# Kernel tuning notes

Measured on AMD Instinct MI355X. Metric: run time of the kernel, lower is better.

The kernel has to match this reference:

```python
import jax, jax.numpy as jnp
import numpy as np
from jax import lax
from jax.scipy.special import logsumexp

B, T, K, D = 16, 128, 1024, 768
APPROX_R = 0.1
LAMBD = 0.1
KP = int(APPROX_R * K)  # num_state_approx = 102


def setup_inputs() -> dict:
    key = jax.random.key(0)
    k0, k1, k2, k3 = jax.random.split(key, 4)
    x_emb = jax.random.normal(k0, (B, T, D), jnp.float32)
    # nn.Parameter(torch.normal(0, norm_scale_transition, [K, D]))
    state_matrix = 0.01 * jax.random.normal(k1, (K, D), jnp.float32)
    y = jax.random.randint(k2, (B, T), 0, K)
    y_lens = jax.random.randint(k3, (B,), 1, T + 1)
    return {"x_emb": x_emb, "state_matrix": state_matrix, "y": y, "y_lens": y_lens}


def _forward_sum(transition, emission, y_lens):
    # exact linear-chain CRF forward (logsumexp) scan. emission: [B,T,K]
    bsz = emission.shape[0]
    def step(alpha, em_t):
        new = logsumexp(alpha[:, :, None] + transition[None], axis=1) + em_t
        return new, new
    a0 = emission[:, 0]
    _, rest = lax.scan(step, a0, jnp.swapaxes(emission, 0, 1)[1:])
    alphas = jnp.concatenate([a0[None], rest], axis=0)  # [T,B,K]
    a_last = alphas[y_lens - 1, jnp.arange(bsz)]        # [B,K]
    return logsumexp(a_last, axis=-1)


def _approx_forward(state_matrix, emission, y_lens, kp):
    # restricted forward over the top-kp states (by emission potential) per
    # position; transitions among selected states computed on the fly from
    # state embeddings (avoids the full KxK transition).
    bsz = emission.shape[0]
    d = state_matrix.shape[1]
    em_top, idx = lax.top_k(emission, kp)   # [B,T,KP]
    st_sel = state_matrix[idx]              # [B,T,KP,D]
    def step(carry, inp):
        alpha, st_prev = carry
        em_t, st_t = inp
        trans_t = jnp.einsum('bid,bjd->bij', st_prev, st_t) / np.sqrt(d)
        new = logsumexp(alpha[:, :, None] + trans_t, axis=1) + em_t
        return (new, st_t), new
    a0 = em_top[:, 0]
    xs = (jnp.swapaxes(em_top, 0, 1)[1:], jnp.swapaxes(st_sel, 0, 1)[1:])
    _, rest = lax.scan(step, (a0, st_sel[:, 0]), xs)
    alphas = jnp.concatenate([a0[None], rest], axis=0)
    a_last = alphas[y_lens - 1, jnp.arange(bsz)]
    return logsumexp(a_last, axis=-1)


def _viterbi(transition, emission, y_lens):
    bsz, tlen, k = emission.shape
    def step(alpha, em_t):
        scores = alpha[:, :, None] + transition[None]
        bp = jnp.argmax(scores, axis=1).astype(jnp.int32)
        new = jnp.max(scores, axis=1) + em_t
        return new, (new, bp)
    a0 = emission[:, 0]
    _, (rest, bps) = lax.scan(step, a0, jnp.swapaxes(emission, 0, 1)[1:])
    alphas = jnp.concatenate([a0[None], rest], axis=0)  # [T,B,K]
    a_last = alphas[y_lens - 1, jnp.arange(bsz)]
    last_state = jnp.argmax(a_last, axis=-1).astype(jnp.int32)
    # bps[t] maps best state at t+1 -> state at t; pad to length T
    bps_pad = jnp.concatenate([bps, jnp.zeros((1, bsz, k), jnp.int32)], axis=0)
    def back(s, inp):
        t, bp_t = inp
        cand = jnp.take_along_axis(bp_t, s[:, None], axis=1)[:, 0]
        s_new = jnp.where(t == y_lens - 1, last_state,
                          jnp.where(t < y_lens - 1, cand, 0))
        return s_new, s_new
    ts = jnp.arange(tlen)[::-1]
    _, s_seq = lax.scan(back, jnp.zeros((bsz,), jnp.int32), (ts, bps_pad[::-1]))
    return jnp.swapaxes(s_seq[::-1], 0, 1)  # [B,T]


def _evaluate(y_pred, y, y_lens, mask_f):
    support = ((y > 0).astype(jnp.float32) * mask_f).sum()
    pred = ((y_pred > 0).astype(jnp.float32) * mask_f).sum()
    overlap = (((y_pred > 0) & (y > 0)).astype(jnp.float32) * mask_f).sum()
    acc = ((y_pred == y).astype(jnp.float32) * mask_f).sum() / y_lens.sum()
    prec = jnp.where(pred > 0, overlap / jnp.maximum(pred, 1.0), 0.0)
    recl = overlap / jnp.maximum(support, 1.0)
    f1 = jnp.where(prec > 0, 2 * prec * recl / jnp.maximum(prec + recl, 1e-12), 0.0)
    return acc, prec, recl, f1


def reference(x_emb, state_matrix, y, y_lens):
    d = x_emb.shape[-1]
    bsz, tlen = y.shape
    emission = jnp.einsum('btd,kd->btk', x_emb, state_matrix) / np.sqrt(d)
    transition = jnp.matmul(state_matrix, state_matrix.T) / np.sqrt(d)

    log_Z = _forward_sum(transition, emission, y_lens)
    log_Z_approx = _approx_forward(state_matrix, emission, y_lens, KP)

    # gold sequence log potential, masked by lengths
    pos = jnp.arange(tlen)
    mask = (pos[None, :] < y_lens[:, None])
    mask_f = mask.astype(jnp.float32)
    mask_tr = (pos[None, :tlen - 1] < (y_lens - 1)[:, None]).astype(jnp.float32)
    em_y = jnp.take_along_axis(emission, y[..., None], axis=-1)[..., 0]
    trans_y = transition[y[:, :-1], y[:, 1:]]
    log_y_potential = (em_y * mask_f).sum(-1) + (trans_y * mask_tr).sum(-1)

    seq_log_prob_exact = -(log_y_potential - log_Z).mean()
    seq_log_prob_approx = -(log_y_potential - log_Z_approx).mean()

    total_len = y_lens.sum()
    logp = jax.nn.log_softmax(emission, axis=-1)
    lp_y = jnp.take_along_axis(logp, y[..., None], axis=-1)[..., 0]
    seq_log_prob_local = (lp_y * mask_f).sum() / total_len
    max_prob = (jnp.max(jax.nn.softmax(emission, -1), -1) * mask_f).sum() / total_len

    # loss_type == 'approx_crf'
    loss = seq_log_prob_approx + LAMBD * seq_log_prob_local

    crf_output = _viterbi(transition, emission, y_lens)
    crf_acc, crf_prec, crf_recl, crf_f1 = _evaluate(crf_output, y, y_lens, mask_f)
    softmax_output = emission.argmax(-1)
    sm_acc, sm_prec, sm_recl, sm_f1 = _evaluate(softmax_output, y, y_lens, mask_f)

    return (loss, crf_output, log_Z.mean(), log_Z_approx.mean(),
            seq_log_prob_exact, seq_log_prob_local, max_prob,
            crf_acc, crf_f1, sm_acc, sm_f1)


if __name__ == '__main__':
    out = reference(**setup_inputs())
    print(out[0], out[2], out[3])
```

## Files before the change

kernel.cpp:

```cpp
#include <hip/hip_runtime.h>
#include <cstdint>
#include <cstddef>

typedef unsigned long long ull;
typedef unsigned int uint32;


#define POISON64 0xFFFFFFFFFFFFFFFFull
#define POISON32 0xFFFFFFFFu

#define OFF_EM    ((size_t)0)
#define OFF_TR    ((size_t)2097152)
#define OFF_EXPTB ((size_t)3145728)
#define OFF_UPP   ((size_t)3670016)
#define OFF_APP   ((size_t)3735552)
#define OFF_ULST  ((size_t)3801088)
#define OFF_ALST  ((size_t)3817472)
#define OFF_UALST ((size_t)3833856)
#define OFF_ETOP  ((size_t)3835904)
#define OFF_ITOP  ((size_t)4044800)
#define OFF_RMAX  ((size_t)4253696)
#define OFF_RLSE  ((size_t)4255744)
#define OFF_SMP   ((size_t)4257792)
#define OFF_BP    ((size_t)4259840)
#define OFF_DONE  ((size_t)6356992)

__device__ __forceinline__ unsigned short f2bf(float f) {
  uint32 u = __builtin_bit_cast(uint32, f);
  u = (u + 0x7fffu + ((u >> 16) & 1u)) >> 16;
  return (unsigned short)u;
}
__device__ __forceinline__ float bflo(uint32 w) {
  return __builtin_bit_cast(float, w << 16);
}
__device__ __forceinline__ float bfhi(uint32 w) {
  return __builtin_bit_cast(float, w & 0xffff0000u);
}

__global__ __launch_bounds__(256) void gemm_kernel(
    const float* __restrict__ x, const float* __restrict__ stm,
    float* __restrict__ emission, float* __restrict__ transition,
    unsigned short* __restrict__ expTb) {
  __shared__ float As[16][68];
  __shared__ float Bs[16][68];
  const int tid = threadIdx.x;
  const int tx = tid & 15, ty = tid >> 4;
  const int m0 = blockIdx.x * 64, n0 = blockIdx.y * 64;
  const int lr = tid >> 2;
  const int lc = (tid & 3) << 2;
  float acc[4][4] = {};
  const float* aptr;
  {
    int gr = m0 + lr;
    aptr = (gr < 2048) ? (x + (size_t)gr * 768) : (stm + (size_t)(gr - 2048) * 768);
  }
  const float* bptr = stm + (size_t)(n0 + lr) * 768;
  for (int k0 = 0; k0 < 768; k0 += 16) {
    float4 a4 = *(const float4*)(aptr + k0 + lc);
    float4 b4 = *(const float4*)(bptr + k0 + lc);
    __syncthreads();
    As[lc + 0][lr] = a4.x; As[lc + 1][lr] = a4.y; As[lc + 2][lr] = a4.z; As[lc + 3][lr] = a4.w;
    Bs[lc + 0][lr] = b4.x; Bs[lc + 1][lr] = b4.y; Bs[lc + 2][lr] = b4.z; Bs[lc + 3][lr] = b4.w;
    __syncthreads();
#pragma unroll
    for (int kk = 0; kk < 16; ++kk) {
      float a[4], b[4];
#pragma unroll
      for (int q = 0; q < 4; ++q) a[q] = As[kk][ty * 4 + q];
#pragma unroll
      for (int q = 0; q < 4; ++q) b[q] = Bs[kk][tx * 4 + q];
#pragma unroll
      for (int i2 = 0; i2 < 4; ++i2)
#pragma unroll
        for (int j2 = 0; j2 < 4; ++j2) acc[i2][j2] += a[i2] * b[j2];
    }
  }
  const float rs = 0.03608439182435161f;
#pragma unroll
  for (int i2 = 0; i2 < 4; ++i2) {
    int r = m0 + ty * 4 + i2;
#pragma unroll
    for (int j2 = 0; j2 < 4; ++j2) {
      int c = n0 + tx * 4 + j2;
      float v = acc[i2][j2] * rs;
      if (r < 2048) {
        emission[(size_t)r * 1024 + c] = v;
      } else {
        size_t o = (size_t)(r - 2048) * 1024 + c;
        transition[o] = v;
        expTb[o] = f2bf(expf(v));
      }
    }
  }
}

__global__ __launch_bounds__(256) void topk_kernel(
    const float* __restrict__ emission, float* __restrict__ em_top,
    int* __restrict__ top_idx, float* __restrict__ row_max,
    float* __restrict__ row_lse, int* __restrict__ sm_pred) {
  __shared__ float v[1024];
  __shared__ int ix[1024];
  __shared__ float rb[256];
  const int row = blockIdx.x;
  const int tid = threadIdx.x;
  const float* e = emission + (size_t)row * 1024;
  for (int p = tid; p < 1024; p += 256) { v[p] = e[p]; ix[p] = p; }
  __syncthreads();
  for (int k = 2; k <= 1024; k <<= 1) {
    for (int j = k >> 1; j > 0; j >>= 1) {
      for (int p = tid; p < 1024; p += 256) {
        int l = p ^ j;
        if (l > p) {
          float va = v[p], vb = v[l];
          int ia = ix[p], ib = ix[l];
          bool aBefore = (va > vb) || (va == vb && ia < ib);
          bool up = ((p & k) == 0);
          if (up ? !aBefore : aBefore) { v[p] = vb; v[l] = va; ix[p] = ib; ix[l] = ia; }
        }
      }
      __syncthreads();
    }
  }
  float mx = v[0];
  float s = 0.f;
  for (int p = tid; p < 1024; p += 256) s += expf(v[p] - mx);
  rb[tid] = s; __syncthreads();
  for (int w = 128; w > 0; w >>= 1) { if (tid < w) rb[tid] += rb[tid + w]; __syncthreads(); }
  if (tid == 0) {
    row_max[row] = mx;
    row_lse[row] = mx + logf(rb[0]);
    sm_pred[row] = ix[0];
  }
  for (int p = tid; p < 102; p += 256) {
    em_top[(size_t)row * 102 + p] = v[p];
    top_idx[(size_t)row * 102 + p] = ix[p];
  }
}

__device__ __forceinline__ void store_bypass2(float* p, float2 v) {
  __hip_atomic_store((ull*)p, __builtin_bit_cast(ull, v),
                     __ATOMIC_RELAXED, __HIP_MEMORY_SCOPE_AGENT);
}
__device__ __forceinline__ void store_bypass_i2(int* p, int2 v) {
  __hip_atomic_store((ull*)p, __builtin_bit_cast(ull, v),
                     __ATOMIC_RELAXED, __HIP_MEMORY_SCOPE_AGENT);
}
__device__ __forceinline__ float load_bypass_f(const float* p) {
  return __hip_atomic_load(p, __ATOMIC_RELAXED, __HIP_MEMORY_SCOPE_AGENT);
}
__device__ __forceinline__ int load_bypass_i(const int* p) {
  return __hip_atomic_load(p, __ATOMIC_RELAXED, __HIP_MEMORY_SCOPE_AGENT);
}
__device__ __forceinline__ void store_bypass_u64(ull* p, ull v) {
  __hip_atomic_store(p, v, __ATOMIC_RELAXED, __HIP_MEMORY_SCOPE_AGENT);
}
__device__ __forceinline__ ull load_bypass_u64(const ull* p) {
  return __hip_atomic_load(p, __ATOMIC_RELAXED, __HIP_MEMORY_SCOPE_AGENT);
}
__device__ __forceinline__ void store_bypass_u32(uint32* p, uint32 v) {
  __hip_atomic_store(p, v, __ATOMIC_RELAXED, __HIP_MEMORY_SCOPE_AGENT);
}
__device__ __forceinline__ uint32 load_bypass_u32(const uint32* p) {
  return __hip_atomic_load(p, __ATOMIC_RELAXED, __HIP_MEMORY_SCOPE_AGENT);
}

__device__ __forceinline__ void stage_poll(const float* __restrict__ src,
                                           float* __restrict__ lds, int tid) {
  const ull* s8 = (const ull*)src;
  ull* l8 = (ull*)lds;
  ull a = load_bypass_u64(s8 + tid);
  ull b = load_bypass_u64(s8 + tid + 256);
  while (a == POISON64) { __builtin_amdgcn_s_sleep(1); a = load_bypass_u64(s8 + tid); }
  while (b == POISON64) { __builtin_amdgcn_s_sleep(1); b = load_bypass_u64(s8 + tid + 256); }
  l8[tid] = a;
  l8[tid + 256] = b;
}

__global__ __launch_bounds__(256) void poison_kernel(
    ull* __restrict__ uring, ull* __restrict__ aring, ull* __restrict__ done) {
  const int idx = blockIdx.x * 256 + threadIdx.x;
  store_bypass_u64(uring + idx, POISON64);
  store_bypass_u64(aring + idx, POISON64);
  if (idx < 1024) store_bypass_u64(done + idx, POISON64);
}

__global__ __launch_bounds__(256, 1) void scan_kernel(
    const float* __restrict__ em, const float* __restrict__ tr,
    const unsigned short* __restrict__ expTb, const float* __restrict__ em_top,
    const int* __restrict__ top_idx, const int* __restrict__ y_lens,
    float* __restrict__ u_ring, float* __restrict__ av_ring,
    float* __restrict__ u_last, float* __restrict__ av_last,
    float* __restrict__ ua_last, int* __restrict__ bp,
    uint32* __restrict__ done, float* __restrict__ out_crf) {
  __shared__ float st[1024];
  __shared__ float psv[896];
  __shared__ int psi[384];
  __shared__ float sua[2][102];
  __shared__ int sidxp[102], sidxc[102];
  __shared__ float aps[102];
  __shared__ float swv[4];
  __shared__ int swi[4];
  const int bid = blockIdx.x, tid = threadIdx.x;

  if (bid < 128) {
    const int b = bid >> 3, s = bid & 7;
    const int tb = y_lens[b] - 1;
    const int tl = tid & 31, h = tid >> 5;
    const int j = s * 128 + tl * 4;
    if (h == 0) {
      const float4 e4 = *(const float4*)(em + (size_t)(b * 128) * 1024 + j);
      float4 v;
      v.x = expf(e4.x); v.y = expf(e4.y); v.z = expf(e4.z); v.w = expf(e4.w);
      float* dst = u_ring + b * 1024 + j;
      store_bypass2(dst, make_float2(v.x, v.y));
      store_bypass2(dst + 2, make_float2(v.z, v.w));
      if (tb == 0) *(float4*)(u_last + b * 1024 + j) = v;
    }
    for (int t = 1; t < 128; ++t) {
      if (tid < 64) {
        if (h == 0) {
          ull* pz = (ull*)(u_ring + (size_t)((t + 2) & 3) * 16384 + b * 1024 + j);
          store_bypass_u64(pz, POISON64);
          store_bypass_u64(pz + 1, POISON64);
        }
        asm volatile("s_waitcnt vmcnt(0)" ::: "memory");
      }
      stage_poll(u_ring + (size_t)((t - 1) & 3) * 16384 + b * 1024, st, tid);
      __syncthreads();
      float a0 = 0.f, a1 = 0.f, a2 = 0.f, a3 = 0.f;
#pragma unroll 4
      for (int i = h * 128; i < h * 128 + 128; ++i) {
        const uint2 w = *(const uint2*)(expTb + (size_t)i * 1024 + j);
        const float ui = st[i];
        a0 += ui * bflo(w.x); a1 += ui * bfhi(w.x);
        a2 += ui * bflo(w.y); a3 += ui * bfhi(w.y);
      }
      if (h) {
        float* p = psv + (h - 1) * 128 + tl * 4;
        p[0] = a0; p[1] = a1; p[2] = a2; p[3] = a3;
      }
      __syncthreads();
      if (h == 0) {
#pragma unroll
        for (int q = 0; q < 7; ++q) {
          const float* p = psv + q * 128 + tl * 4;
          a0 += p[0]; a1 += p[1]; a2 += p[2]; a3 += p[3];
        }
        const float4 e4 = *(const float4*)(em + ((size_t)b * 128 + t) * 1024 + j);
        float4 v;
        v.x = a0 * expf(e4.x) * (1.0f / 1024.0f);
        v.y = a1 * expf(e4.y) * (1.0f / 1024.0f);
        v.z = a2 * expf(e4.z) * (1.0f / 1024.0f);
        v.w = a3 * expf(e4.w) * (1.0f / 1024.0f);
        float* dst = u_ring + (size_t)(t & 3) * 16384 + b * 1024 + j;
        store_bypass2(dst, make_float2(v.x, v.y));
        store_bypass2(dst + 2, make_float2(v.z, v.w));
        if (t == tb) *(float4*)(u_last + b * 1024 + j) = v;
      }
    }
  } else if (bid < 256) {
    const int local = bid - 128;
    const int b = local >> 3, s = local & 7;
    const int tb = y_lens[b] - 1;
    const int tl = tid & 63, h = tid >> 6;
    const int j = s * 128 + tl * 2;
    if (h == 0) {
      const float2 e2 = *(const float2*)(em + (size_t)(b * 128) * 1024 + j);
      store_bypass2(av_ring + b * 1024 + j, e2);
      if (tb == 0) store_bypass2(av_last + b * 1024 + j, e2);
    }
    for (int t = 1; t < 128; ++t) {
      if (tid < 64) {
        ull* pz = (ull*)(av_ring + (size_t)((t + 2) & 3) * 16384 + b * 1024 + j);
        store_bypass_u64(pz, POISON64);
        asm volatile("s_waitcnt vmcnt(0)" ::: "memory");
      }
      stage_poll(av_ring + (size_t)((t - 1) & 3) * 16384 + b * 1024, st, tid);
      __syncthreads();
      float m0 = -3.0e38f, m1 = -3.0e38f;
      int x0 = 0x7fffffff, x1 = 0x7fffffff;
#pragma unroll 4
      for (int i = h * 256; i < h * 256 + 256; ++i) {
        const float2 t2 = *(const float2*)(tr + (size_t)i * 1024 + j);
        const float ai = st[i];
        float c0 = ai + t2.x;
        float c1 = ai + t2.y;
        if (c0 > m0) { m0 = c0; x0 = i; }
        if (c1 > m1) { m1 = c1; x1 = i; }
      }
      if (h) {
        psv[(h - 1) * 128 + tl * 2] = m0; psv[(h - 1) * 128 + tl * 2 + 1] = m1;
        psi[(h - 1) * 128 + tl * 2] = x0; psi[(h - 1) * 128 + tl * 2 + 1] = x1;
      }
      __syncthreads();
      if (h == 0) {
#pragma unroll
        for (int q = 0; q < 3; ++q) {
          float p0 = psv[q * 128 + tl * 2], p1 = psv[q * 128 + tl * 2 + 1];
          int y0 = psi[q * 128 + tl * 2], y1 = psi[q * 128 + tl * 2 + 1];
          if (p0 > m0) { m0 = p0; x0 = y0; }
          if (p1 > m1) { m1 = p1; x1 = y1; }
        }
        const float2 e2 = *(const float2*)(em + ((size_t)b * 128 + t) * 1024 + j);
        float2 nv = make_float2(m0 + e2.x, m1 + e2.y);
        store_bypass2(av_ring + (size_t)(t & 3) * 16384 + b * 1024 + j, nv);
        store_bypass_i2(bp + (size_t)t * 16384 + b * 1024 + j, make_int2(x0, x1));
        if (t == tb) store_bypass2(av_last + b * 1024 + j, nv);
      }
    }
    if (tid == 0) {
      asm volatile("s_waitcnt vmcnt(0)" ::: "memory");
      store_bypass_u32(done + (size_t)(b * 8 + s) * 16, 0u);
    }
    if (s == 0) {
      if (tid < 8) {
        const uint32* dp = done + (size_t)(b * 8 + tid) * 16;
        while (load_bypass_u32(dp) == POISON32) __builtin_amdgcn_s_sleep(1);
      }
      __syncthreads();
      const int tbb = tb;
      for (int t2 = tbb + 1 + tid; t2 < 128; t2 += 256) out_crf[b * 128 + t2] = 0.f;
      const float* al = av_last + b * 1024;
      float bv = -3.0e38f;
      int bi = 0x7fffffff;
      for (int i = tid; i < 1024; i += 256) {
        float val = load_bypass_f(al + i);
        if (val > bv || (val == bv && i < bi)) { bv = val; bi = i; }
      }
      for (int off = 32; off > 0; off >>= 1) {
        float ov = __shfl_xor(bv, off);
        int oi = __shfl_xor(bi, off);
        if (ov > bv || (ov == bv && oi < bi)) { bv = ov; bi = oi; }
      }
      if ((tid & 63) == 0) { swv[tid >> 6] = bv; swi[tid >> 6] = bi; }
      __syncthreads();
      if (tid == 0) {
        for (int q = 1; q < 4; ++q)
          if (swv[q] > bv || (swv[q] == bv && swi[q] < bi)) { bv = swv[q]; bi = swi[q]; }
        int sx = bi;
        out_crf[b * 128 + tbb] = (float)sx;
        for (int t2 = tbb - 1; t2 >= 0; --t2) {
          sx = load_bypass_i(bp + (size_t)(t2 + 1) * 16384 + b * 1024 + sx);
          out_crf[b * 128 + t2] = (float)sx;
        }
      }
    }
  } else {
    const int b = bid - 256;
    const int tb = y_lens[b] - 1;
    const int j2 = tid & 127, h2 = tid >> 7;
    if (tid < 102) {
      float v = expf(em_top[(size_t)(b * 128) * 102 + tid]);
      sua[0][tid] = v;
      if (tb == 0) ua_last[b * 102 + tid] = v;
    }
    __syncthreads();
    for (int t = 1; t < 128; ++t) {
      if (tid < 102) {
        sidxp[tid] = top_idx[((size_t)b * 128 + (t - 1)) * 102 + tid];
        sidxc[tid] = top_idx[((size_t)b * 128 + t) * 102 + tid];
      }
      __syncthreads();
      float acc2 = 0.f;
      if (j2 < 102) {
        const int col = sidxc[j2];
        const float* up = sua[(t - 1) & 1];
        for (int i = h2 * 51; i < h2 * 51 + 51; ++i)
          acc2 += up[i] * bflo((uint32)expTb[(size_t)sidxp[i] * 1024 + col]);
      }
      if (h2 == 1 && j2 < 102) aps[j2] = acc2;
      __syncthreads();
      if (h2 == 0 && j2 < 102) {
        acc2 += aps[j2];
        float e = em_top[((size_t)b * 128 + t) * 102 + j2];
        float nv = acc2 * expf(e) * (1.0f / 102.0f);
        sua[t & 1][j2] = nv;
        if (t == tb) ua_last[b * 102 + j2] = nv;
      }
      __syncthreads();
    }
  }
}

__device__ __forceinline__ float blk_sum(float v, float* rb, int tid) {
  rb[tid] = v; __syncthreads();
  for (int w = 128; w > 0; w >>= 1) { if (tid < w) rb[tid] += rb[tid + w]; __syncthreads(); }
  float r = rb[0]; __syncthreads();
  return r;
}

__global__ __launch_bounds__(256) void finalize_kernel(
    const float* __restrict__ emission, const float* __restrict__ transition,
    const float* __restrict__ u_last, const float* __restrict__ ua_last,
    const float* __restrict__ row_max, const float* __restrict__ row_lse,
    const int* __restrict__ sm_pred, const int* __restrict__ y,
    const int* __restrict__ y_lens, float* __restrict__ d_out) {
  __shared__ float rb[256];
  __shared__ float sZ[16], sZa[16], sLogy[16];
  const int tid = threadIdx.x;
  const float* out_crf = d_out + 1;
  for (int b = 0; b < 16; ++b) {
    const int tb = y_lens[b] - 1;
    float p = 0.f;
    for (int i = tid; i < 1024; i += 256) p += u_last[(size_t)b * 1024 + i];
    p = blk_sum(p, rb, tid);
    if (tid == 0) sZ[b] = logf(p) + (float)tb * 6.931471805599453f;
    float q = 0.f;
    for (int i = tid; i < 102; i += 256) q += ua_last[(size_t)b * 102 + i];
    q = blk_sum(q, rb, tid);
    if (tid == 0) sZa[b] = logf(q) + (float)tb * 4.624972813284271f;
  }
  if (tid < 16) sLogy[tid] = 0.f;
  __syncthreads();
  float a_local = 0, a_maxp = 0, c_sup = 0, c_pred = 0, c_ov = 0, c_match = 0;
  float s_predc = 0, s_ov = 0, s_match = 0;
  for (int r = tid; r < 2048; r += 256) {
    const int b = r >> 7, t = r & 127;
    const int L = y_lens[b];
    if (t < L) {
      const int yv = y[r];
      const float em_y = emission[(size_t)r * 1024 + yv];
      const float lse = row_lse[r];
      a_local += em_y - lse;
      a_maxp += expf(row_max[r] - lse);
      float term = em_y;
      if (t < L - 1) term += transition[(size_t)yv * 1024 + y[r + 1]];
      atomicAdd(&sLogy[b], term);
      const float ypos = (yv > 0) ? 1.f : 0.f;
      c_sup += ypos;
      const int cs = (int)out_crf[r];
      c_pred += (cs > 0) ? 1.f : 0.f;
      c_ov += ((cs > 0) && (yv > 0)) ? 1.f : 0.f;
      c_match += (cs == yv) ? 1.f : 0.f;
      const int ss = sm_pred[r];
      s_predc += (ss > 0) ? 1.f : 0.f;
      s_ov += ((ss > 0) && (yv > 0)) ? 1.f : 0.f;
      s_match += (ss == yv) ? 1.f : 0.f;
    }
  }
  __syncthreads();
  a_local = blk_sum(a_local, rb, tid);
  a_maxp = blk_sum(a_maxp, rb, tid);
  c_sup = blk_sum(c_sup, rb, tid);
  c_pred = blk_sum(c_pred, rb, tid);
  c_ov = blk_sum(c_ov, rb, tid);
  c_match = blk_sum(c_match, rb, tid);
  s_predc = blk_sum(s_predc, rb, tid);
  s_ov = blk_sum(s_ov, rb, tid);
  s_match = blk_sum(s_match, rb, tid);
  if (tid == 0) {
    float tl = 0.f;
    for (int b = 0; b < 16; ++b) tl += (float)y_lens[b];
    float mZ = 0, mZa = 0, dE = 0, dA = 0;
    for (int b = 0; b < 16; ++b) {
      mZ += sZ[b]; mZa += sZa[b];
      dE += sLogy[b] - sZ[b];
      dA += sLogy[b] - sZa[b];
    }
    mZ *= (1.f / 16.f); mZa *= (1.f / 16.f);
    const float sle = -dE * (1.f / 16.f);
    const float sla = -dA * (1.f / 16.f);
    const float slocal = a_local / tl;
    const float maxp = a_maxp / tl;
    const float loss = sla + 0.1f * slocal;
    const float crf_acc = c_match / tl;
    const float crf_prec = (c_pred > 0.f) ? (c_ov / fmaxf(c_pred, 1.f)) : 0.f;
    const float crf_recl = c_ov / fmaxf(c_sup, 1.f);
    const float crf_f1 = (crf_prec > 0.f)
        ? (2.f * crf_prec * crf_recl / fmaxf(crf_prec + crf_recl, 1e-12f)) : 0.f;
    const float sm_acc = s_match / tl;
    const float sm_prec = (s_predc > 0.f) ? (s_ov / fmaxf(s_predc, 1.f)) : 0.f;
    const float sm_recl = s_ov / fmaxf(c_sup, 1.f);
    const float sm_f1 = (sm_prec > 0.f)
        ? (2.f * sm_prec * sm_recl / fmaxf(sm_prec + sm_recl, 1e-12f)) : 0.f;
    d_out[0] = loss;
    d_out[2049] = mZ;
    d_out[2050] = mZa;
    d_out[2051] = sle;
    d_out[2052] = slocal;
    d_out[2053] = maxp;
    d_out[2054] = crf_acc;
    d_out[2055] = crf_f1;
    d_out[2056] = sm_acc;
    d_out[2057] = sm_f1;
  }
}

extern "C" void kernel_launch(void* const* d_in, const int* in_sizes, int n_in,
                              void* d_out, int out_size, void* d_ws, size_t ws_size,
                              hipStream_t stream) {
  const float* x = (const float*)d_in[0];
  const float* stm = (const float*)d_in[1];
  const int* y = (const int*)d_in[2];
  const int* yl = (const int*)d_in[3];
  float* out = (float*)d_out;
  float* ws = (float*)d_ws;

  float* emission = ws + OFF_EM;
  float* transition = ws + OFF_TR;
  unsigned short* expTb = (unsigned short*)(ws + OFF_EXPTB);
  float* u_ring = ws + OFF_UPP;
  float* av_ring = ws + OFF_APP;
  float* u_last = ws + OFF_ULST;
  float* av_last = ws + OFF_ALST;
  float* ua_last = ws + OFF_UALST;
  float* em_top = ws + OFF_ETOP;
  int* top_idx = (int*)(ws + OFF_ITOP);
  float* row_max = ws + OFF_RMAX;
  float* row_lse = ws + OFF_RLSE;
  int* sm_pred = (int*)(ws + OFF_SMP);
  int* bp = (int*)(ws + OFF_BP);
  uint32* done = (uint32*)(ws + OFF_DONE);

  poison_kernel<<<128, 256, 0, stream>>>((ull*)u_ring, (ull*)av_ring, (ull*)done);
  gemm_kernel<<<dim3(48, 16), 256, 0, stream>>>(x, stm, emission, transition, expTb);
  topk_kernel<<<2048, 256, 0, stream>>>(emission, em_top, top_idx, row_max, row_lse, sm_pred);
  scan_kernel<<<272, 256, 0, stream>>>(emission, transition, expTb, em_top, top_idx,
                                       yl, u_ring, av_ring, u_last, av_last, ua_last,
                                       bp, done, out + 1);
  finalize_kernel<<<1, 256, 0, stream>>>(emission, transition, u_last, ua_last,
                                         row_max, row_lse, sm_pred, y, yl, out);
}
```

Baseline: 1.914 ms.

## Batch forward scan across sequences with split-bf16 MFMA and restructured Viterbi blocks

Recasts the exact forward recursion as a batched 16x1024 by 1024x1024 product per step, with all 16 sequences handled together across 8 blocks. It uses bf16 MFMA on a transposed exp-transition matrix and splits alpha into high and low bf16 parts to keep accuracy. The Viterbi path is repartitioned so each of 128 blocks covers 8 columns for all batches, and signalling moves from poisoned data rings to per-block sentinel flags. Block count drops and threads per block double. This adds a transpose kernel and more cross-block synchronization, and increases precision risk on the rescaled forward values.

```diff
diff --git a/kernel.cpp b/kernel.cpp
--- a/kernel.cpp
+++ b/kernel.cpp
@@ -4,10 +4,13 @@
 
 typedef unsigned long long ull;
 typedef unsigned int uint32;
-
-
+typedef unsigned short u16;
+typedef __attribute__((ext_vector_type(8))) short s8v;
+typedef __attribute__((ext_vector_type(4))) float f32x4;
+
+
+#define POISON32 0xFFFFFFFFu
 #define POISON64 0xFFFFFFFFFFFFFFFFull
-#define POISON32 0xFFFFFFFFu
 
 #define OFF_EM    ((size_t)0)
 #define OFF_TR    ((size_t)2097152)
@@ -24,23 +27,57 @@
 #define OFF_SMP   ((size_t)4257792)
 #define OFF_BP    ((size_t)4259840)
 #define OFF_DONE  ((size_t)6356992)
-
-__device__ __forceinline__ unsigned short f2bf(float f) {
+#define OFF_EXPTT ((size_t)6367744)
+
+__device__ __forceinline__ u16 f2bf(float f) {
   uint32 u = __builtin_bit_cast(uint32, f);
   u = (u + 0x7fffu + ((u >> 16) & 1u)) >> 16;
-  return (unsigned short)u;
+  return (u16)u;
 }
 __device__ __forceinline__ float bflo(uint32 w) {
   return __builtin_bit_cast(float, w << 16);
 }
 __device__ __forceinline__ float bfhi(uint32 w) {
   return __builtin_bit_cast(float, w & 0xffff0000u);
+}
+__device__ __forceinline__ void bfsplit(float v, u16& h, u16& l) {
+  h = f2bf(v);
+  float rh = __builtin_bit_cast(float, ((uint32)h) << 16);
+  l = f2bf(v - rh);
+}
+
+__device__ __forceinline__ ull load_bypass_u64(const ull* p) {
+  return __hip_atomic_load(p, __ATOMIC_RELAXED, __HIP_MEMORY_SCOPE_AGENT);
+}
+__device__ __forceinline__ void store_bypass_u64(ull* p, ull v) {
+  __hip_atomic_store(p, v, __ATOMIC_RELAXED, __HIP_MEMORY_SCOPE_AGENT);
+}
+__device__ __forceinline__ uint32 load_bypass_u32(const uint32* p) {
+  return __hip_atomic_load(p, __ATOMIC_RELAXED, __HIP_MEMORY_SCOPE_AGENT);
+}
+__device__ __forceinline__ void store_bypass_u32(uint32* p, uint32 v) {
+  __hip_atomic_store(p, v, __ATOMIC_RELAXED, __HIP_MEMORY_SCOPE_AGENT);
+}
+__device__ __forceinline__ void store_bypass_u16(u16* p, u16 v) {
+  __hip_atomic_store(p, v, __ATOMIC_RELAXED, __HIP_MEMORY_SCOPE_AGENT);
+}
+__device__ __forceinline__ float load_bypass_f(const float* p) {
+  return __hip_atomic_load(p, __ATOMIC_RELAXED, __HIP_MEMORY_SCOPE_AGENT);
+}
+__device__ __forceinline__ void store_bypass_f(float* p, float v) {
+  __hip_atomic_store(p, v, __ATOMIC_RELAXED, __HIP_MEMORY_SCOPE_AGENT);
+}
+__device__ __forceinline__ void store_bypass_i(int* p, int v) {
+  __hip_atomic_store(p, v, __ATOMIC_RELAXED, __HIP_MEMORY_SCOPE_AGENT);
+}
+__device__ __forceinline__ int load_bypass_i(const int* p) {
+  return __hip_atomic_load(p, __ATOMIC_RELAXED, __HIP_MEMORY_SCOPE_AGENT);
 }
 
 __global__ __launch_bounds__(256) void gemm_kernel(
     const float* __restrict__ x, const float* __restrict__ stm,
     float* __restrict__ emission, float* __restrict__ transition,
-    unsigned short* __restrict__ expTb) {
+    u16* __restrict__ expTb) {
   __shared__ float As[16][68];
   __shared__ float Bs[16][68];
   const int tid = threadIdx.x;
@@ -92,6 +129,18 @@
       }
     }
   }
+}
+
+__global__ __launch_bounds__(256) void transT_kernel(
+    const u16* __restrict__ src, u16* __restrict__ dst) {
+  __shared__ u16 tile[64][65];
+  const int bx = blockIdx.x * 64, by = blockIdx.y * 64;
+  const int tx = threadIdx.x & 63, ty4 = threadIdx.x >> 6;
+  for (int rr = ty4; rr < 64; rr += 4)
+    tile[rr][tx] = src[(size_t)(bx + rr) * 1024 + by + tx];
+  __syncthreads();
+  for (int rr = ty4; rr < 64; rr += 4)
+    dst[(size_t)(by + rr) * 1024 + bx + tx] = tile[tx][rr];
 }
 
 __global__ __launch_bounds__(256) void topk_kernel(
@@ -137,244 +186,302 @@
   }
 }
 
-__device__ __forceinline__ void store_bypass2(float* p, float2 v) {
-  __hip_atomic_store((ull*)p, __builtin_bit_cast(ull, v),
-                     __ATOMIC_RELAXED, __HIP_MEMORY_SCOPE_AGENT);
-}
-__device__ __forceinline__ void store_bypass_i2(int* p, int2 v) {
-  __hip_atomic_store((ull*)p, __builtin_bit_cast(ull, v),
-                     __ATOMIC_RELAXED, __HIP_MEMORY_SCOPE_AGENT);
-}
-__device__ __forceinline__ float load_bypass_f(const float* p) {
-  return __hip_atomic_load(p, __ATOMIC_RELAXED, __HIP_MEMORY_SCOPE_AGENT);
-}
-__device__ __forceinline__ int load_bypass_i(const int* p) {
-  return __hip_atomic_load(p, __ATOMIC_RELAXED, __HIP_MEMORY_SCOPE_AGENT);
-}
-__device__ __forceinline__ void store_bypass_u64(ull* p, ull v) {
-  __hip_atomic_store(p, v, __ATOMIC_RELAXED, __HIP_MEMORY_SCOPE_AGENT);
-}
-__device__ __forceinline__ ull load_bypass_u64(const ull* p) {
-  return __hip_atomic_load(p, __ATOMIC_RELAXED, __HIP_MEMORY_SCOPE_AGENT);
-}
-__device__ __forceinline__ void store_bypass_u32(uint32* p, uint32 v) {
-  __hip_atomic_store(p, v, __ATOMIC_RELAXED, __HIP_MEMORY_SCOPE_AGENT);
-}
-__device__ __forceinline__ uint32 load_bypass_u32(const uint32* p) {
-  return __hip_atomic_load(p, __ATOMIC_RELAXED, __HIP_MEMORY_SCOPE_AGENT);
-}
-
-__device__ __forceinline__ void stage_poll(const float* __restrict__ src,
-                                           float* __restrict__ lds, int tid) {
-  const ull* s8 = (const ull*)src;
-  ull* l8 = (ull*)lds;
-  ull a = load_bypass_u64(s8 + tid);
-  ull b = load_bypass_u64(s8 + tid + 256);
-  while (a == POISON64) { __builtin_amdgcn_s_sleep(1); a = load_bypass_u64(s8 + tid); }
-  while (b == POISON64) { __builtin_amdgcn_s_sleep(1); b = load_bypass_u64(s8 + tid + 256); }
-  l8[tid] = a;
-  l8[tid + 256] = b;
-}
-
-__global__ __launch_bounds__(256) void poison_kernel(
-    ull* __restrict__ uring, ull* __restrict__ aring, ull* __restrict__ done) {
+__global__ __launch_bounds__(256) void poison_kernel(ull* __restrict__ done8) {
   const int idx = blockIdx.x * 256 + threadIdx.x;
-  store_bypass_u64(uring + idx, POISON64);
-  store_bypass_u64(aring + idx, POISON64);
-  if (idx < 1024) store_bypass_u64(done + idx, POISON64);
-}
-
-__global__ __launch_bounds__(256, 1) void scan_kernel(
+  store_bypass_u64(done8 + idx, POISON64);
+}
+
+__global__ __launch_bounds__(512) void scan_kernel(
     const float* __restrict__ em, const float* __restrict__ tr,
-    const unsigned short* __restrict__ expTb, const float* __restrict__ em_top,
-    const int* __restrict__ top_idx, const int* __restrict__ y_lens,
+    const u16* __restrict__ expTb, const u16* __restrict__ expTbT,
+    const float* __restrict__ em_top, const int* __restrict__ top_idx,
+    const int* __restrict__ y_lens,
     float* __restrict__ u_ring, float* __restrict__ av_ring,
     float* __restrict__ u_last, float* __restrict__ av_last,
     float* __restrict__ ua_last, int* __restrict__ bp,
     uint32* __restrict__ done, float* __restrict__ out_crf) {
-  __shared__ float st[1024];
-  __shared__ float psv[896];
-  __shared__ int psi[384];
-  __shared__ float sua[2][102];
-  __shared__ int sidxp[102], sidxc[102];
-  __shared__ float aps[102];
-  __shared__ float swv[4];
-  __shared__ int swi[4];
+  __shared__ ull SH[9232];
   const int bid = blockIdx.x, tid = threadIdx.x;
-
-  if (bid < 128) {
-    const int b = bid >> 3, s = bid & 7;
-    const int tb = y_lens[b] - 1;
-    const int tl = tid & 31, h = tid >> 5;
-    const int j = s * 128 + tl * 4;
-    if (h == 0) {
-      const float4 e4 = *(const float4*)(em + (size_t)(b * 128) * 1024 + j);
-      float4 v;
-      v.x = expf(e4.x); v.y = expf(e4.y); v.z = expf(e4.z); v.w = expf(e4.w);
-      float* dst = u_ring + b * 1024 + j;
-      store_bypass2(dst, make_float2(v.x, v.y));
-      store_bypass2(dst + 2, make_float2(v.z, v.w));
-      if (tb == 0) *(float4*)(u_last + b * 1024 + j) = v;
-    }
-    for (int t = 1; t < 128; ++t) {
-      if (tid < 64) {
-        if (h == 0) {
-          ull* pz = (ull*)(u_ring + (size_t)((t + 2) & 3) * 16384 + b * 1024 + j);
-          store_bypass_u64(pz, POISON64);
-          store_bypass_u64(pz + 1, POISON64);
-        }
-        asm volatile("s_waitcnt vmcnt(0)" ::: "memory");
-      }
-      stage_poll(u_ring + (size_t)((t - 1) & 3) * 16384 + b * 1024, st, tid);
-      __syncthreads();
-      float a0 = 0.f, a1 = 0.f, a2 = 0.f, a3 = 0.f;
-#pragma unroll 4
-      for (int i = h * 128; i < h * 128 + 128; ++i) {
-        const uint2 w = *(const uint2*)(expTb + (size_t)i * 1024 + j);
-        const float ui = st[i];
-        a0 += ui * bflo(w.x); a1 += ui * bfhi(w.x);
-        a2 += ui * bflo(w.y); a3 += ui * bfhi(w.y);
-      }
-      if (h) {
-        float* p = psv + (h - 1) * 128 + tl * 4;
-        p[0] = a0; p[1] = a1; p[2] = a2; p[3] = a3;
-      }
-      __syncthreads();
-      if (h == 0) {
-#pragma unroll
-        for (int q = 0; q < 7; ++q) {
-          const float* p = psv + q * 128 + tl * 4;
-          a0 += p[0]; a1 += p[1]; a2 += p[2]; a3 += p[3];
-        }
-        const float4 e4 = *(const float4*)(em + ((size_t)b * 128 + t) * 1024 + j);
-        float4 v;
-        v.x = a0 * expf(e4.x) * (1.0f / 1024.0f);
-        v.y = a1 * expf(e4.y) * (1.0f / 1024.0f);
-        v.z = a2 * expf(e4.z) * (1.0f / 1024.0f);
-        v.w = a3 * expf(e4.w) * (1.0f / 1024.0f);
-        float* dst = u_ring + (size_t)(t & 3) * 16384 + b * 1024 + j;
-        store_bypass2(dst, make_float2(v.x, v.y));
-        store_bypass2(dst + 2, make_float2(v.z, v.w));
-        if (t == tb) *(float4*)(u_last + b * 1024 + j) = v;
-      }
-    }
-  } else if (bid < 256) {
-    const int local = bid - 128;
-    const int b = local >> 3, s = local & 7;
-    const int tb = y_lens[b] - 1;
-    const int tl = tid & 63, h = tid >> 6;
-    const int j = s * 128 + tl * 2;
-    if (h == 0) {
-      const float2 e2 = *(const float2*)(em + (size_t)(b * 128) * 1024 + j);
-      store_bypass2(av_ring + b * 1024 + j, e2);
-      if (tb == 0) store_bypass2(av_last + b * 1024 + j, e2);
-    }
-    for (int t = 1; t < 128; ++t) {
-      if (tid < 64) {
-        ull* pz = (ull*)(av_ring + (size_t)((t + 2) & 3) * 16384 + b * 1024 + j);
-        store_bypass_u64(pz, POISON64);
-        asm volatile("s_waitcnt vmcnt(0)" ::: "memory");
-      }
-      stage_poll(av_ring + (size_t)((t - 1) & 3) * 16384 + b * 1024, st, tid);
-      __syncthreads();
-      float m0 = -3.0e38f, m1 = -3.0e38f;
-      int x0 = 0x7fffffff, x1 = 0x7fffffff;
-#pragma unroll 4
-      for (int i = h * 256; i < h * 256 + 256; ++i) {
-        const float2 t2 = *(const float2*)(tr + (size_t)i * 1024 + j);
-        const float ai = st[i];
-        float c0 = ai + t2.x;
-        float c1 = ai + t2.y;
-        if (c0 > m0) { m0 = c0; x0 = i; }
-        if (c1 > m1) { m1 = c1; x1 = i; }
-      }
-      if (h) {
-        psv[(h - 1) * 128 + tl * 2] = m0; psv[(h - 1) * 128 + tl * 2 + 1] = m1;
-        psi[(h - 1) * 128 + tl * 2] = x0; psi[(h - 1) * 128 + tl * 2 + 1] = x1;
-      }
-      __syncthreads();
-      if (h == 0) {
-#pragma unroll
-        for (int q = 0; q < 3; ++q) {
-          float p0 = psv[q * 128 + tl * 2], p1 = psv[q * 128 + tl * 2 + 1];
-          int y0 = psi[q * 128 + tl * 2], y1 = psi[q * 128 + tl * 2 + 1];
-          if (p0 > m0) { m0 = p0; x0 = y0; }
-          if (p1 > m1) { m1 = p1; x1 = y1; }
-        }
-        const float2 e2 = *(const float2*)(em + ((size_t)b * 128 + t) * 1024 + j);
-        float2 nv = make_float2(m0 + e2.x, m1 + e2.y);
-        store_bypass2(av_ring + (size_t)(t & 3) * 16384 + b * 1024 + j, nv);
-        store_bypass_i2(bp + (size_t)t * 16384 + b * 1024 + j, make_int2(x0, x1));
-        if (t == tb) store_bypass2(av_last + b * 1024 + j, nv);
-      }
-    }
+  uint32* sentF = done;
+  uint32* sentV = done + 512;
+  uint32* vdone = done + 8704;
+
+  if (bid < 8) {
+    const int p = bid;
+    int* stbF = (int*)(SH + 8192);
+    if (tid < 16) stbF[tid] = y_lens[tid] - 1;
+    const int l = tid & 63;
+    const int lm = l & 15, lq = l >> 4;
+    const int w2 = (tid >> 6) & 3;
+    if (tid < 256) {
+      const int m = tid >> 4;
+      const int nn = p * 128 + ((tid & 15) << 3);
+      const float* e0 = em + ((size_t)m << 17) + nn;
+      u16* rh = (u16*)u_ring;
+      const bool last0 = (y_lens[m] == 1);
+#pragma unroll
+      for (int q = 0; q < 8; ++q) {
+        float v = expf(e0[q]);
+        u16 h, lo2; bfsplit(v, h, lo2);
+        store_bypass_u16(rh + m * 1024 + nn + q, h);
+        store_bypass_u16(rh + 16384 + m * 1024 + nn + q, lo2);
+        if (last0) u_last[(size_t)m * 1024 + nn + q] = v;
+      }
+    }
+    __syncthreads();
     if (tid == 0) {
       asm volatile("s_waitcnt vmcnt(0)" ::: "memory");
-      store_bypass_u32(done + (size_t)(b * 8 + s) * 16, 0u);
-    }
-    if (s == 0) {
+      store_bypass_u32(sentF + p * 16, 0u);
+    }
+    const char* Ab = (const char*)SH;
+    const int offh = (lm << 11) + (lq << 4);
+    const int axor = (lm & 7) << 4;
+    const int nbase = p * 128 + w2 * 32;
+    const u16* bq0 = expTbT + ((size_t)(nbase + lm) << 10) + (lq << 3);
+    const u16* bq1 = bq0 + (16 << 10);
+    for (int t = 1; t < 128; ++t) {
       if (tid < 8) {
-        const uint32* dp = done + (size_t)(b * 8 + tid) * 16;
-        while (load_bypass_u32(dp) == POISON32) __builtin_amdgcn_s_sleep(1);
-      }
-      __syncthreads();
-      const int tbb = tb;
-      for (int t2 = tbb + 1 + tid; t2 < 128; t2 += 256) out_crf[b * 128 + t2] = 0.f;
-      const float* al = av_last + b * 1024;
-      float bv = -3.0e38f;
-      int bi = 0x7fffffff;
-      for (int i = tid; i < 1024; i += 256) {
-        float val = load_bypass_f(al + i);
+        const uint32* sp = sentF + (size_t)((t - 1) & 3) * 128 + tid * 16;
+        while (load_bypass_u32(sp) == POISON32) __builtin_amdgcn_s_sleep(1);
+      }
+      __syncthreads();
+      if (tid == 0)
+        store_bypass_u32(sentF + (size_t)((t + 2) & 3) * 128 + p * 16, POISON32);
+      {
+        const ull* src = (const ull*)(u_ring + (size_t)((t - 1) & 3) * 16384);
+        ull dbuf[16];
+#pragma unroll
+        for (int q = 0; q < 16; ++q) dbuf[q] = load_bypass_u64(src + tid + (q << 9));
+#pragma unroll
+        for (int q = 0; q < 16; ++q) {
+          const int ob = (tid + (q << 9)) << 3;
+          *(ull*)((char*)SH + (ob ^ (((ob >> 11) & 7) << 4))) = dbuf[q];
+        }
+      }
+      __syncthreads();
+      if (tid < 256) {
+        f32x4 acc0a = {0.f, 0.f, 0.f, 0.f}, acc0b = {0.f, 0.f, 0.f, 0.f};
+        f32x4 acc1a = {0.f, 0.f, 0.f, 0.f}, acc1b = {0.f, 0.f, 0.f, 0.f};
+        for (int k0 = 0; k0 < 1024; k0 += 64) {
+          const int o0 = (offh + (k0 << 1)) ^ axor;
+          const int o1 = (offh + ((k0 + 32) << 1)) ^ axor;
+          s8v ah0 = *(const s8v*)(Ab + o0);
+          s8v al0 = *(const s8v*)(Ab + 32768 + o0);
+          s8v ah1 = *(const s8v*)(Ab + o1);
+          s8v al1 = *(const s8v*)(Ab + 32768 + o1);
+          s8v b00 = *(const s8v*)(bq0 + k0);
+          s8v b10 = *(const s8v*)(bq1 + k0);
+          s8v b01 = *(const s8v*)(bq0 + k0 + 32);
+          s8v b11 = *(const s8v*)(bq1 + k0 + 32);
+          acc0a = __builtin_amdgcn_mfma_f32_16x16x32_bf16(ah0, b00, acc0a, 0, 0, 0);
+          acc1a = __builtin_amdgcn_mfma_f32_16x16x32_bf16(ah0, b10, acc1a, 0, 0, 0);
+          acc0b = __builtin_amdgcn_mfma_f32_16x16x32_bf16(ah1, b01, acc0b, 0, 0, 0);
+          acc1b = __builtin_amdgcn_mfma_f32_16x16x32_bf16(ah1, b11, acc1b, 0, 0, 0);
+          acc0a = __builtin_amdgcn_mfma_f32_16x16x32_bf16(al0, b00, acc0a, 0, 0, 0);
+          acc1a = __builtin_amdgcn_mfma_f32_16x16x32_bf16(al0, b10, acc1a, 0, 0, 0);
+          acc0b = __builtin_amdgcn_mfma_f32_16x16x32_bf16(al1, b01, acc0b, 0, 0, 0);
+          acc1b = __builtin_amdgcn_mfma_f32_16x16x32_bf16(al1, b11, acc1b, 0, 0, 0);
+        }
+        u16* rh = (u16*)(u_ring + (size_t)(t & 3) * 16384);
+        const float sc = 1.0f / 1024.0f;
+#pragma unroll
+        for (int r = 0; r < 4; ++r) {
+          const int m = (lq << 2) + r;
+          const size_t erow = (((size_t)m << 7) + t) << 10;
+          {
+            const int n = nbase + lm;
+            float v = (acc0a[r] + acc0b[r]) * sc * expf(em[erow + n]);
+            u16 h, lo2; bfsplit(v, h, lo2);
+            store_bypass_u16(rh + m * 1024 + n, h);
+            store_bypass_u16(rh + 16384 + m * 1024 + n, lo2);
+            if (t == stbF[m]) u_last[(size_t)m * 1024 + n] = v;
+          }
+          {
+            const int n = nbase + 16 + lm;
+            float v = (acc1a[r] + acc1b[r]) * sc * expf(em[erow + n]);
+            u16 h, lo2; bfsplit(v, h, lo2);
+            store_bypass_u16(rh + m * 1024 + n, h);
+            store_bypass_u16(rh + 16384 + m * 1024 + n, lo2);
+            if (t == stbF[m]) u_last[(size_t)m * 1024 + n] = v;
+          }
+        }
+        asm volatile("s_waitcnt vmcnt(0)" ::: "memory");
+      }
+      __syncthreads();
+      if (tid == 0) store_bypass_u32(sentF + (size_t)(t & 3) * 128 + p * 16, 0u);
+    }
+  } else if (bid < 136) {
+    const int v = bid - 8;
+    const int n0v = ((v & 7) << 7) + ((v >> 3) << 3);
+    const int jj = tid & 7, g = tid >> 3;
+    const int col = n0v + jj;
+    ull* ppb = (ull*)((char*)SH + 65536);
+    int* stb2 = (int*)((char*)SH + 73728);
+    if (tid < 16) stb2[tid] = y_lens[tid] - 1;
+    if (tid < 128) {
+      const int jb = tid & 7, b = tid >> 3;
+      const float e0 = em[((size_t)b << 17) + n0v + jb];
+      store_bypass_f(av_ring + (size_t)(n0v + jb) * 16 + b, e0);
+      if (y_lens[b] == 1) store_bypass_f(av_last + ((size_t)b << 10) + n0v + jb, e0);
+    }
+    __syncthreads();
+    if (tid == 0) {
+      asm volatile("s_waitcnt vmcnt(0)" ::: "memory");
+      store_bypass_u32(sentV + v * 16, 0u);
+    }
+    const char* stc = (const char*)SH;
+    for (int t = 1; t < 128; ++t) {
+      if (tid < 128) {
+        const uint32* sp = sentV + (size_t)((t - 1) & 3) * 2048 + tid * 16;
+        while (load_bypass_u32(sp) == POISON32) __builtin_amdgcn_s_sleep(1);
+      }
+      __syncthreads();
+      if (tid == 0)
+        store_bypass_u32(sentV + (size_t)((t + 2) & 3) * 2048 + v * 16, POISON32);
+      {
+        const ull* src = (const ull*)(av_ring + (size_t)((t - 1) & 3) * 16384);
+        ull dbuf[16];
+#pragma unroll
+        for (int q = 0; q < 16; ++q) dbuf[q] = load_bypass_u64(src + tid + (q << 9));
+#pragma unroll
+        for (int q = 0; q < 16; ++q) {
+          const int ob = (tid + (q << 9)) << 3;
+          *(ull*)((char*)SH + (ob ^ (((ob >> 10) & 7) << 4))) = dbuf[q];
+        }
+      }
+      __syncthreads();
+      float mv[16]; int mi[16];
+#pragma unroll
+      for (int b = 0; b < 16; ++b) { mv[b] = -3.0e38f; mi[b] = 0x7fffffff; }
+      const float* trc = tr + col;
+      const int i0 = g << 4;
+#pragma unroll 4
+      for (int ii = 0; ii < 16; ++ii) {
+        const int i = i0 + ii;
+        const float tv = trc[(size_t)i << 10];
+        const int ph = (i << 6) ^ (((i >> 4) & 7) << 4);
+        const f32x4 s0 = *(const f32x4*)(stc + (ph ^ 0));
+        const f32x4 s1 = *(const f32x4*)(stc + (ph ^ 16));
+        const f32x4 s2 = *(const f32x4*)(stc + (ph ^ 32));
+        const f32x4 s3 = *(const f32x4*)(stc + (ph ^ 48));
+#pragma unroll
+        for (int b = 0; b < 4; ++b) {
+          float c0 = s0[b] + tv; if (c0 > mv[b])      { mv[b] = c0;      mi[b] = i; }
+          float c1 = s1[b] + tv; if (c1 > mv[b + 4])  { mv[b + 4] = c1;  mi[b + 4] = i; }
+          float c2 = s2[b] + tv; if (c2 > mv[b + 8])  { mv[b + 8] = c2;  mi[b + 8] = i; }
+          float c3 = s3[b] + tv; if (c3 > mv[b + 12]) { mv[b + 12] = c3; mi[b + 12] = i; }
+        }
+      }
+#pragma unroll
+      for (int d = 8; d <= 32; d <<= 1) {
+#pragma unroll
+        for (int b = 0; b < 16; ++b) {
+          float ov = __shfl_xor(mv[b], d);
+          int oi = __shfl_xor(mi[b], d);
+          if (ov > mv[b] || (ov == mv[b] && oi < mi[b])) { mv[b] = ov; mi[b] = oi; }
+        }
+      }
+      if ((tid & 63) < 8) {
+        const int wv = tid >> 6;
+#pragma unroll
+        for (int b = 0; b < 16; ++b) {
+          ull pk = ((ull)(uint32)mi[b] << 32) | (ull)__builtin_bit_cast(uint32, mv[b]);
+          ppb[(b << 6) + (wv << 3) + jj] = pk;
+        }
+      }
+      __syncthreads();
+      if (tid < 128) {
+        const int jb = tid & 7, b = tid >> 3;
+        const int cf = n0v + jb;
+        float bmv = -3.0e38f; int bmi = 0x7fffffff;
+#pragma unroll
+        for (int w = 0; w < 8; ++w) {
+          ull pk = ppb[(b << 6) + (w << 3) + jb];
+          float pv = __builtin_bit_cast(float, (uint32)pk);
+          int pi = (int)(pk >> 32);
+          if (pv > bmv || (pv == bmv && pi < bmi)) { bmv = pv; bmi = pi; }
+        }
+        const float nv = bmv + em[((((size_t)b << 7) + t) << 10) + cf];
+        store_bypass_f(av_ring + (size_t)(t & 3) * 16384 + (size_t)cf * 16 + b, nv);
+        store_bypass_i(bp + ((size_t)t << 14) + ((size_t)b << 10) + cf, bmi);
+        if (t == stb2[b]) store_bypass_f(av_last + ((size_t)b << 10) + cf, nv);
+        asm volatile("s_waitcnt vmcnt(0)" ::: "memory");
+      }
+      __syncthreads();
+      if (tid == 0) store_bypass_u32(sentV + (size_t)(t & 3) * 2048 + v * 16, 0u);
+    }
+    if (tid == 0) {
+      asm volatile("s_waitcnt vmcnt(0)" ::: "memory");
+      store_bypass_u32(vdone + v * 16, 0u);
+    }
+    if (v == 0) {
+      if (tid < 128) {
+        while (load_bypass_u32(vdone + tid * 16) == POISON32) __builtin_amdgcn_s_sleep(1);
+      }
+      __syncthreads();
+      const int wv = tid >> 6, lh = tid & 63;
+      const int hb = lh >> 5, hl = lh & 31;
+      const int b = wv * 2 + hb;
+      const int tbb = y_lens[b] - 1;
+      for (int t2 = tbb + 1 + hl; t2 < 128; t2 += 32) out_crf[(b << 7) + t2] = 0.f;
+      float bv = -3.0e38f; int bi = 0x7fffffff;
+      for (int q = 0; q < 32; ++q) {
+        const int i = (q << 5) + hl;
+        const float val = load_bypass_f(av_last + ((size_t)b << 10) + i);
         if (val > bv || (val == bv && i < bi)) { bv = val; bi = i; }
       }
-      for (int off = 32; off > 0; off >>= 1) {
-        float ov = __shfl_xor(bv, off);
-        int oi = __shfl_xor(bi, off);
+#pragma unroll
+      for (int d = 1; d < 32; d <<= 1) {
+        float ov = __shfl_xor(bv, d, 32);
+        int oi = __shfl_xor(bi, d, 32);
         if (ov > bv || (ov == bv && oi < bi)) { bv = ov; bi = oi; }
       }
-      if ((tid & 63) == 0) { swv[tid >> 6] = bv; swi[tid >> 6] = bi; }
-      __syncthreads();
-      if (tid == 0) {
-        for (int q = 1; q < 4; ++q)
-          if (swv[q] > bv || (swv[q] == bv && swi[q] < bi)) { bv = swv[q]; bi = swi[q]; }
+      if (hl == 0) {
         int sx = bi;
-        out_crf[b * 128 + tbb] = (float)sx;
+        out_crf[(b << 7) + tbb] = (float)sx;
         for (int t2 = tbb - 1; t2 >= 0; --t2) {
-          sx = load_bypass_i(bp + (size_t)(t2 + 1) * 16384 + b * 1024 + sx);
-          out_crf[b * 128 + t2] = (float)sx;
+          sx = load_bypass_i(bp + ((size_t)(t2 + 1) << 14) + ((size_t)b << 10) + sx);
+          out_crf[(b << 7) + t2] = (float)sx;
         }
       }
     }
   } else {
-    const int b = bid - 256;
+    const int b = bid - 136;
     const int tb = y_lens[b] - 1;
     const int j2 = tid & 127, h2 = tid >> 7;
+    float* sua0 = (float*)SH;
+    float* sua1 = sua0 + 104;
+    int* sidxp = (int*)(sua0 + 208);
+    int* sidxc = sidxp + 104;
+    float* aps = (float*)(sidxc + 104);
     if (tid < 102) {
-      float v = expf(em_top[(size_t)(b * 128) * 102 + tid]);
-      sua[0][tid] = v;
-      if (tb == 0) ua_last[b * 102 + tid] = v;
+      float vv = expf(em_top[(size_t)(b * 128) * 102 + tid]);
+      sua0[tid] = vv;
+      if (tb == 0) ua_last[b * 102 + tid] = vv;
     }
     __syncthreads();
     for (int t = 1; t < 128; ++t) {
-      if (tid < 102) {
-        sidxp[tid] = top_idx[((size_t)b * 128 + (t - 1)) * 102 + tid];
-        sidxc[tid] = top_idx[((size_t)b * 128 + t) * 102 + tid];
-      }
+      if (tid < 102) sidxp[tid] = top_idx[((size_t)b * 128 + (t - 1)) * 102 + tid];
+      else if (tid >= 256 && tid < 358)
+        sidxc[tid - 256] = top_idx[((size_t)b * 128 + t) * 102 + (tid - 256)];
       __syncthreads();
       float acc2 = 0.f;
+      float* up = (t & 1) ? sua0 : sua1;
+      float* cur = (t & 1) ? sua1 : sua0;
       if (j2 < 102) {
-        const int col = sidxc[j2];
-        const float* up = sua[(t - 1) & 1];
-        for (int i = h2 * 51; i < h2 * 51 + 51; ++i)
-          acc2 += up[i] * bflo((uint32)expTb[(size_t)sidxp[i] * 1024 + col]);
-      }
-      if (h2 == 1 && j2 < 102) aps[j2] = acc2;
+        const int colc = sidxc[j2];
+        const int ia = h2 * 26;
+        const int ib2 = (ia + 26 < 102) ? ia + 26 : 102;
+        for (int i = ia; i < ib2; ++i)
+          acc2 += up[i] * bflo((uint32)expTb[(size_t)sidxp[i] * 1024 + colc]);
+      }
+      if (h2 > 0 && j2 < 102) aps[(h2 - 1) * 104 + j2] = acc2;
       __syncthreads();
       if (h2 == 0 && j2 < 102) {
-        acc2 += aps[j2];
-        float e = em_top[((size_t)b * 128 + t) * 102 + j2];
-        float nv = acc2 * expf(e) * (1.0f / 102.0f);
-        sua[t & 1][j2] = nv;
+        acc2 += aps[j2] + aps[104 + j2] + aps[208 + j2];
+        const float e = em_top[((size_t)b * 128 + t) * 102 + j2];
+        const float nv = acc2 * expf(e) * (1.0f / 102.0f);
+        cur[j2] = nv;
         if (t == tb) ua_last[b * 102 + j2] = nv;
       }
       __syncthreads();
@@ -498,7 +605,8 @@
 
   float* emission = ws + OFF_EM;
   float* transition = ws + OFF_TR;
-  unsigned short* expTb = (unsigned short*)(ws + OFF_EXPTB);
+  u16* expTb = (u16*)(ws + OFF_EXPTB);
+  u16* expTbT = (u16*)(ws + OFF_EXPTT);
   float* u_ring = ws + OFF_UPP;
   float* av_ring = ws + OFF_APP;
   float* u_last = ws + OFF_ULST;
@@ -512,10 +620,11 @@
   int* bp = (int*)(ws + OFF_BP);
   uint32* done = (uint32*)(ws + OFF_DONE);
 
-  poison_kernel<<<128, 256, 0, stream>>>((ull*)u_ring, (ull*)av_ring, (ull*)done);
+  poison_kernel<<<21, 256, 0, stream>>>((ull*)done);
   gemm_kernel<<<dim3(48, 16), 256, 0, stream>>>(x, stm, emission, transition, expTb);
+  transT_kernel<<<dim3(16, 16), 256, 0, stream>>>(expTb, expTbT);
   topk_kernel<<<2048, 256, 0, stream>>>(emission, em_top, top_idx, row_max, row_lse, sm_pred);
-  scan_kernel<<<272, 256, 0, stream>>>(emission, transition, expTb, em_top, top_idx,
+  scan_kernel<<<152, 512, 0, stream>>>(emission, transition, expTb, expTbT, em_top, top_idx,
                                        yl, u_ring, av_ring, u_last, av_last, ua_last,
                                        bp, done, out + 1);
   finalize_kernel<<<1, 256, 0, stream>>>(emission, transition, u_last, ua_last,
```

Measured after the change: 1.914 ms. About the same (-0.0%).
